# Performance work log

Hardware: AMD Instinct MI355X
Metric: run time of the kernel (lower is better)

Reference implementation:

```python
import jax, jax.numpy as jnp
import numpy as np

B, S, D, H = 64, 512, 1024, 1024


def setup_inputs() -> dict:
    key = jax.random.key(0)
    ks = jax.random.split(key, 7)
    stdv = 1.0 / np.sqrt(H)
    u = lambda k, shape: jax.random.uniform(k, shape, jnp.float32, -stdv, stdv)
    return {
        "inputs": jax.random.normal(ks[0], (B, S, D), jnp.float32),
        "h0": jax.random.normal(ks[1], (1, B, H), jnp.float32),
        "c0": jax.random.normal(ks[2], (1, B, H), jnp.float32),
        "weight_ih": u(ks[3], (4 * H, D)),
        "weight_hh": u(ks[4], (4 * H, H)),
        "bias_ih": u(ks[5], (4 * H,)),
        "bias_hh": u(ks[6], (4 * H,)),
    }


def reference(inputs, h0, c0, weight_ih, weight_hh, bias_ih, bias_hh):
    # Precompute input projection for all timesteps: [B, S, 4H]
    x_proj = jnp.einsum("bsd,gd->bsg", inputs, weight_ih) + bias_ih

    def step(carry, xp):
        h, c = carry  # [B, H]
        gates = xp + h @ weight_hh.T + bias_hh  # [B, 4H]
        i, f, g, o = jnp.split(gates, 4, axis=-1)  # torch gate order: i, f, g(c), o
        i = jax.nn.sigmoid(i)
        f = jax.nn.sigmoid(f)
        g = jnp.tanh(g)
        o = jax.nn.sigmoid(o)
        c = f * c + i * g
        h = o * jnp.tanh(c)
        return (h, c), h

    (hn, cn), outs = jax.lax.scan(step, (h0[0], c0[0]), jnp.swapaxes(x_proj, 0, 1))
    outputs = jnp.swapaxes(outs, 0, 1)  # [B, S, H]
    return outputs, hn[None], cn[None]
```

## Files before the change

### kernel.cpp

```cpp
#include <hip/hip_runtime.h>

typedef __bf16 bf16x8 __attribute__((ext_vector_type(8)));
typedef float f32x4 __attribute__((ext_vector_type(4)));

#define T_STEPS 512

__device__ __forceinline__ float fsig(float v) { return 1.0f / (1.0f + __expf(-v)); }
__device__ __forceinline__ float ftanhf(float v) {
    float a = fminf(fmaxf(v, -15.0f), 15.0f);
    float e = __expf(2.0f * a);
    return (e - 1.0f) / (e + 1.0f);
}
__device__ __forceinline__ unsigned short f2bfu(float f) {
    unsigned u = __float_as_uint(f);
    u += 0x7fffu + ((u >> 16) & 1u);
    return (unsigned short)(u >> 16);
}
__device__ __forceinline__ bf16x8 cvt8(float4 a, float4 b) {
    bf16x8 f;
    f[0] = (__bf16)a.x; f[1] = (__bf16)a.y; f[2] = (__bf16)a.z; f[3] = (__bf16)a.w;
    f[4] = (__bf16)b.x; f[5] = (__bf16)b.y; f[6] = (__bf16)b.z; f[7] = (__bf16)b.w;
    return f;
}

__device__ __forceinline__ void load_hb8(const unsigned short* p, uint4* f) {
    asm volatile(
        "global_load_dwordx4 %0, %8, off sc0 sc1\n\t"
        "global_load_dwordx4 %1, %8, off offset:64 sc0 sc1\n\t"
        "global_load_dwordx4 %2, %8, off offset:128 sc0 sc1\n\t"
        "global_load_dwordx4 %3, %8, off offset:192 sc0 sc1\n\t"
        "global_load_dwordx4 %4, %8, off offset:256 sc0 sc1\n\t"
        "global_load_dwordx4 %5, %8, off offset:320 sc0 sc1\n\t"
        "global_load_dwordx4 %6, %8, off offset:384 sc0 sc1\n\t"
        "global_load_dwordx4 %7, %8, off offset:448 sc0 sc1\n\t"
        "s_waitcnt vmcnt(0)"
        : "=&v"(f[0]), "=&v"(f[1]), "=&v"(f[2]), "=&v"(f[3]),
          "=&v"(f[4]), "=&v"(f[5]), "=&v"(f[6]), "=&v"(f[7])
        : "v"(p)
        : "memory");
}
__device__ __forceinline__ void store_hb(unsigned short* p, unsigned short v) {
    unsigned int vv = v;
    asm volatile("global_store_short %0, %1, off sc0 sc1"
                 :: "v"(p), "v"(vv) : "memory");
}
__device__ __forceinline__ void vm_drain() {
    asm volatile("s_waitcnt vmcnt(0)" ::: "memory");
}

__global__ __launch_bounds__(512, 2) void lstm_persist(
    const float* __restrict__ x, const float* __restrict__ h0,
    const float* __restrict__ c0, const float* __restrict__ w_ih,
    const float* __restrict__ w_hh, const float* __restrict__ b_ih,
    const float* __restrict__ b_hh, float* __restrict__ out,
    unsigned short* __restrict__ hb, int* __restrict__ arrive)
{
    const int tid  = threadIdx.x;
    const int wave = tid >> 6;
    const int lane = tid & 63;
    const int bid  = blockIdx.x;
    const int bg   = bid >> 6;
    const int cg   = bid & 63;
    const int colbase = cg << 4;
    const int batbase = bg << 4;

    __shared__ float xred[2][4][4][4][64];
    __shared__ float hred[4][4][4][64];

    const int quad = lane >> 4;
    const int l15  = lane & 15;

    bf16x8 bw[8][4];
    {
        const float* wsrc = (wave < 4) ? w_ih : w_hh;
        const int koff = (wave & 3) * 256 + quad * 8;
        #pragma unroll
        for (int n = 0; n < 4; ++n) {
            const float* prow = wsrc + (size_t)((n << 10) + colbase + l15) * 1024 + koff;
            #pragma unroll
            for (int kk = 0; kk < 8; ++kk) {
                float4 a = *(const float4*)(prow + kk * 32);
                float4 b = *(const float4*)(prow + kk * 32 + 4);
                bw[kk][n] = cvt8(a, b);
            }
        }
    }

    float creg = 0.0f, bias0 = 0.f, bias1 = 0.f, bias2 = 0.f, bias3 = 0.f;
    int cellcolg = 0, cellb = 0;
    if (tid < 256) {
        const int cl = tid & 63;
        const int cv = tid >> 6;
        const int cellrow = ((cl >> 4) << 2) + cv;
        cellcolg = colbase + (cl & 15);
        cellb    = batbase + cellrow;
        creg  = c0[cellb * 1024 + cellcolg];
        bias0 = b_ih[cellcolg]        + b_hh[cellcolg];
        bias1 = b_ih[1024 + cellcolg] + b_hh[1024 + cellcolg];
        bias2 = b_ih[2048 + cellcolg] + b_hh[2048 + cellcolg];
        bias3 = b_ih[3072 + cellcolg] + b_hh[3072 + cellcolg];
    }

    float* outp = out;
    float* hnp  = out + (size_t)64 * 512 * 1024;
    float* cnp  = hnp + 64 * 1024;

    const int abatch = batbase + l15;

    float4 pa[8], pb[8];

    if (wave < 4) {
        const float* px = x + ((size_t)abatch * 512 + 0) * 1024 + wave * 256 + quad * 8;
        f32x4 xacc[4];
        #pragma unroll
        for (int n = 0; n < 4; ++n) xacc[n] = (f32x4){0.f, 0.f, 0.f, 0.f};
        #pragma unroll
        for (int kk = 0; kk < 8; ++kk) {
            float4 a = *(const float4*)(px + kk * 32);
            float4 b = *(const float4*)(px + kk * 32 + 4);
            bf16x8 af = cvt8(a, b);
            xacc[0] = __builtin_amdgcn_mfma_f32_16x16x32_bf16(af, bw[kk][0], xacc[0], 0, 0, 0);
            xacc[1] = __builtin_amdgcn_mfma_f32_16x16x32_bf16(af, bw[kk][1], xacc[1], 0, 0, 0);
            xacc[2] = __builtin_amdgcn_mfma_f32_16x16x32_bf16(af, bw[kk][2], xacc[2], 0, 0, 0);
            xacc[3] = __builtin_amdgcn_mfma_f32_16x16x32_bf16(af, bw[kk][3], xacc[3], 0, 0, 0);
        }
        #pragma unroll
        for (int n = 0; n < 4; ++n)
            #pragma unroll
            for (int v = 0; v < 4; ++v)
                xred[0][wave][n][v][lane] = xacc[n][v];
        const float* pn = x + ((size_t)abatch * 512 + 1) * 1024 + wave * 256 + quad * 8;
        #pragma unroll
        for (int kk = 0; kk < 8; ++kk) {
            pa[kk] = *(const float4*)(pn + kk * 32);
            pb[kk] = *(const float4*)(pn + kk * 32 + 4);
        }
    }

    for (int t = 0; t < T_STEPS; ++t) {
        if (wave >= 4) {
            f32x4 acc[4];
            #pragma unroll
            for (int n = 0; n < 4; ++n) acc[n] = (f32x4){0.f, 0.f, 0.f, 0.f};

            if (t == 0) {
                const float* ph = h0 + abatch * 1024 + (wave & 3) * 256 + quad * 8;
                #pragma unroll
                for (int kk = 0; kk < 8; ++kk) {
                    float4 a = *(const float4*)(ph + kk * 32);
                    float4 b = *(const float4*)(ph + kk * 32 + 4);
                    bf16x8 af = cvt8(a, b);
                    acc[0] = __builtin_amdgcn_mfma_f32_16x16x32_bf16(af, bw[kk][0], acc[0], 0, 0, 0);
                    acc[1] = __builtin_amdgcn_mfma_f32_16x16x32_bf16(af, bw[kk][1], acc[1], 0, 0, 0);
                    acc[2] = __builtin_amdgcn_mfma_f32_16x16x32_bf16(af, bw[kk][2], acc[2], 0, 0, 0);
                    acc[3] = __builtin_amdgcn_mfma_f32_16x16x32_bf16(af, bw[kk][3], acc[3], 0, 0, 0);
                }
            } else {
                const int* slot = &arrive[(bg << 6) + lane];
                while (__hip_atomic_load(slot, __ATOMIC_RELAXED,
                                         __HIP_MEMORY_SCOPE_AGENT) < t) {
                    __builtin_amdgcn_s_sleep(1);
                }
                const unsigned short* ph = hb + ((t - 1) & 1) * 65536
                                             + abatch * 1024 + (wave & 3) * 256 + quad * 8;
                uint4 fr[8];
                load_hb8(ph, fr);
                #pragma unroll
                for (int kk = 0; kk < 8; ++kk) {
                    union { uint4 u; bf16x8 v; } cc;
                    cc.u = fr[kk];
                    acc[0] = __builtin_amdgcn_mfma_f32_16x16x32_bf16(cc.v, bw[kk][0], acc[0], 0, 0, 0);
                    acc[1] = __builtin_amdgcn_mfma_f32_16x16x32_bf16(cc.v, bw[kk][1], acc[1], 0, 0, 0);
                    acc[2] = __builtin_amdgcn_mfma_f32_16x16x32_bf16(cc.v, bw[kk][2], acc[2], 0, 0, 0);
                    acc[3] = __builtin_amdgcn_mfma_f32_16x16x32_bf16(cc.v, bw[kk][3], acc[3], 0, 0, 0);
                }
            }
            #pragma unroll
            for (int n = 0; n < 4; ++n)
                #pragma unroll
                for (int v = 0; v < 4; ++v)
                    hred[wave - 4][n][v][lane] = acc[n][v];
        }

        __syncthreads();

        float hval = 0.f;
        if (tid < 256) {
            const int cl = tid & 63;
            const int cv = tid >> 6;
            float g0 = bias0, g1 = bias1, g2 = bias2, g3 = bias3;
            #pragma unroll
            for (int w = 0; w < 4; ++w) {
                g0 += xred[t & 1][w][0][cv][cl] + hred[w][0][cv][cl];
                g1 += xred[t & 1][w][1][cv][cl] + hred[w][1][cv][cl];
                g2 += xred[t & 1][w][2][cv][cl] + hred[w][2][cv][cl];
                g3 += xred[t & 1][w][3][cv][cl] + hred[w][3][cv][cl];
            }
            float ig = fsig(g0), fg = fsig(g1), gg = ftanhf(g2), og = fsig(g3);
            creg = fg * creg + ig * gg;
            hval = og * ftanhf(creg);
            store_hb(hb + (t & 1) * 65536 + cellb * 1024 + cellcolg, f2bfu(hval));
            vm_drain();
        }

        __syncthreads();

        if (tid == 0 && t < T_STEPS - 1)
            __hip_atomic_store(&arrive[bid], t + 1, __ATOMIC_RELAXED,
                               __HIP_MEMORY_SCOPE_AGENT);

        if (wave < 4) {
            outp[((size_t)cellb * 512 + t) * 1024 + cellcolg] = hval;
            if (t == T_STEPS - 1) {
                hnp[cellb * 1024 + cellcolg] = hval;
                cnp[cellb * 1024 + cellcolg] = creg;
            }
            if (t < T_STEPS - 1) {
                f32x4 xacc[4];
                #pragma unroll
                for (int n = 0; n < 4; ++n) xacc[n] = (f32x4){0.f, 0.f, 0.f, 0.f};
                #pragma unroll
                for (int kk = 0; kk < 8; ++kk) {
                    bf16x8 af = cvt8(pa[kk], pb[kk]);
                    xacc[0] = __builtin_amdgcn_mfma_f32_16x16x32_bf16(af, bw[kk][0], xacc[0], 0, 0, 0);
                    xacc[1] = __builtin_amdgcn_mfma_f32_16x16x32_bf16(af, bw[kk][1], xacc[1], 0, 0, 0);
                    xacc[2] = __builtin_amdgcn_mfma_f32_16x16x32_bf16(af, bw[kk][2], xacc[2], 0, 0, 0);
                    xacc[3] = __builtin_amdgcn_mfma_f32_16x16x32_bf16(af, bw[kk][3], xacc[3], 0, 0, 0);
                }
                #pragma unroll
                for (int n = 0; n < 4; ++n)
                    #pragma unroll
                    for (int v = 0; v < 4; ++v)
                        xred[(t + 1) & 1][wave][n][v][lane] = xacc[n][v];
                if (t + 2 < T_STEPS) {
                    const float* pn = x + ((size_t)abatch * 512 + (t + 2)) * 1024
                                        + wave * 256 + quad * 8;
                    #pragma unroll
                    for (int kk = 0; kk < 8; ++kk) {
                        pa[kk] = *(const float4*)(pn + kk * 32);
                        pb[kk] = *(const float4*)(pn + kk * 32 + 4);
                    }
                }
            }
        }
    }
}

extern "C" void kernel_launch(void* const* d_in, const int* in_sizes, int n_in,
                              void* d_out, int out_size, void* d_ws, size_t ws_size,
                              hipStream_t stream) {
    const float* x   = (const float*)d_in[0];
    const float* h0  = (const float*)d_in[1];
    const float* c0  = (const float*)d_in[2];
    const float* wih = (const float*)d_in[3];
    const float* whh = (const float*)d_in[4];
    const float* bih = (const float*)d_in[5];
    const float* bhh = (const float*)d_in[6];
    float* out = (float*)d_out;
    unsigned short* hb = (unsigned short*)d_ws;
    int* arrive = (int*)((char*)d_ws + 2 * 65536 * sizeof(unsigned short));
    hipLaunchKernelGGL(lstm_persist, dim3(256), dim3(512), 0, stream,
                       x, h0, c0, wih, whh, bih, bhh, out, hb, arrive);
}
```

Measured before the change: 4.146 ms.

## Replace per-block arrival flags with per-batch-group atomic counter and LDS go flag

Cross-block synchronisation moves from 64 per-block arrival slots, polled by every lane of four waves, to one atomic counter per batch group. Each cell wave increments it after publishing h, and a single wave polls it, then releases the other waves through an LDS flag. The cell update moves to the h-waves so the second __syncthreads before signaling is removed, and the x-waves read h back from LDS to write the outputs. This cuts global polling traffic and shortens the critical path between steps, but adds atomics contention and relies on a memset of the counter before launch.

```diff
diff --git a/kernel.cpp b/kernel.cpp
--- a/kernel.cpp
+++ b/kernel.cpp
@@ -53,7 +53,7 @@
     const float* __restrict__ c0, const float* __restrict__ w_ih,
     const float* __restrict__ w_hh, const float* __restrict__ b_ih,
     const float* __restrict__ b_hh, float* __restrict__ out,
-    unsigned short* __restrict__ hb, int* __restrict__ arrive)
+    unsigned short* __restrict__ hb, int* __restrict__ cnt_base)
 {
     const int tid  = threadIdx.x;
     const int wave = tid >> 6;
@@ -65,10 +65,14 @@
     const int batbase = bg << 4;
 
     __shared__ float xred[2][4][4][4][64];
-    __shared__ float hred[4][4][4][64];
+    __shared__ float hredLDS[4][4][4][64];
+    __shared__ float hout[256];
+    __shared__ int go;
 
     const int quad = lane >> 4;
     const int l15  = lane & 15;
+
+    int* cnt = cnt_base + (bg << 5);
 
     bf16x8 bw[8][4];
     {
@@ -86,20 +90,21 @@
         }
     }
 
+    const int cv = (tid >> 6) & 3;
+    const int cellrow  = ((lane >> 4) << 2) + cv;
+    const int cellcolg = colbase + l15;
+    const int cellb    = batbase + cellrow;
+
     float creg = 0.0f, bias0 = 0.f, bias1 = 0.f, bias2 = 0.f, bias3 = 0.f;
-    int cellcolg = 0, cellb = 0;
-    if (tid < 256) {
-        const int cl = tid & 63;
-        const int cv = tid >> 6;
-        const int cellrow = ((cl >> 4) << 2) + cv;
-        cellcolg = colbase + (cl & 15);
-        cellb    = batbase + cellrow;
+    if (wave >= 4) {
         creg  = c0[cellb * 1024 + cellcolg];
         bias0 = b_ih[cellcolg]        + b_hh[cellcolg];
         bias1 = b_ih[1024 + cellcolg] + b_hh[1024 + cellcolg];
         bias2 = b_ih[2048 + cellcolg] + b_hh[2048 + cellcolg];
         bias3 = b_ih[3072 + cellcolg] + b_hh[3072 + cellcolg];
     }
+    if (tid == 256) __hip_atomic_store(&go, 0, __ATOMIC_RELAXED,
+                                       __HIP_MEMORY_SCOPE_WORKGROUP);
 
     float* outp = out;
     float* hnp  = out + (size_t)64 * 512 * 1024;
@@ -156,10 +161,25 @@
                     acc[3] = __builtin_amdgcn_mfma_f32_16x16x32_bf16(af, bw[kk][3], acc[3], 0, 0, 0);
                 }
             } else {
-                const int* slot = &arrive[(bg << 6) + lane];
-                while (__hip_atomic_load(slot, __ATOMIC_RELAXED,
-                                         __HIP_MEMORY_SCOPE_AGENT) < t) {
-                    __builtin_amdgcn_s_sleep(1);
+                const int target = t << 8;
+                if (wave == 4) {
+                    for (;;) {
+                        int p = 0;
+                        if (lane == 0)
+                            p = __hip_atomic_load(cnt, __ATOMIC_RELAXED,
+                                                  __HIP_MEMORY_SCOPE_AGENT);
+                        p = __builtin_amdgcn_readfirstlane(p);
+                        if (p >= target) break;
+                        __builtin_amdgcn_s_sleep(1);
+                    }
+                    if (lane == 0)
+                        __hip_atomic_store(&go, t, __ATOMIC_RELAXED,
+                                           __HIP_MEMORY_SCOPE_WORKGROUP);
+                } else {
+                    while (__hip_atomic_load(&go, __ATOMIC_RELAXED,
+                                             __HIP_MEMORY_SCOPE_WORKGROUP) < t) {
+                        __builtin_amdgcn_s_sleep(1);
+                    }
                 }
                 const unsigned short* ph = hb + ((t - 1) & 1) * 65536
                                              + abatch * 1024 + (wave & 3) * 256 + quad * 8;
@@ -179,42 +199,43 @@
             for (int n = 0; n < 4; ++n)
                 #pragma unroll
                 for (int v = 0; v < 4; ++v)
-                    hred[wave - 4][n][v][lane] = acc[n][v];
+                    hredLDS[wave - 4][n][v][lane] = acc[n][v];
         }
 
         __syncthreads();
 
-        float hval = 0.f;
-        if (tid < 256) {
-            const int cl = tid & 63;
-            const int cv = tid >> 6;
+        if (wave >= 4) {
+            const int v = wave - 4;
             float g0 = bias0, g1 = bias1, g2 = bias2, g3 = bias3;
+            const int buf = t & 1;
             #pragma unroll
             for (int w = 0; w < 4; ++w) {
-                g0 += xred[t & 1][w][0][cv][cl] + hred[w][0][cv][cl];
-                g1 += xred[t & 1][w][1][cv][cl] + hred[w][1][cv][cl];
-                g2 += xred[t & 1][w][2][cv][cl] + hred[w][2][cv][cl];
-                g3 += xred[t & 1][w][3][cv][cl] + hred[w][3][cv][cl];
+                g0 += xred[buf][w][0][v][lane] + hredLDS[w][0][v][lane];
+                g1 += xred[buf][w][1][v][lane] + hredLDS[w][1][v][lane];
+                g2 += xred[buf][w][2][v][lane] + hredLDS[w][2][v][lane];
+                g3 += xred[buf][w][3][v][lane] + hredLDS[w][3][v][lane];
             }
             float ig = fsig(g0), fg = fsig(g1), gg = ftanhf(g2), og = fsig(g3);
             creg = fg * creg + ig * gg;
-            hval = og * ftanhf(creg);
+            float hval = og * ftanhf(creg);
+            hout[(v << 6) + lane] = hval;
             store_hb(hb + (t & 1) * 65536 + cellb * 1024 + cellcolg, f2bfu(hval));
-            vm_drain();
-        }
-
-        __syncthreads();
-
-        if (tid == 0 && t < T_STEPS - 1)
-            __hip_atomic_store(&arrive[bid], t + 1, __ATOMIC_RELAXED,
-                               __HIP_MEMORY_SCOPE_AGENT);
-
-        if (wave < 4) {
-            outp[((size_t)cellb * 512 + t) * 1024 + cellcolg] = hval;
             if (t == T_STEPS - 1) {
                 hnp[cellb * 1024 + cellcolg] = hval;
                 cnp[cellb * 1024 + cellcolg] = creg;
-            }
+            } else {
+                vm_drain();
+                if (lane == 0)
+                    __hip_atomic_fetch_add(cnt, 1, __ATOMIC_RELAXED,
+                                           __HIP_MEMORY_SCOPE_AGENT);
+            }
+        }
+
+        __syncthreads();
+
+        if (wave < 4) {
+            float hval = hout[tid];
+            outp[((size_t)cellb * 512 + t) * 1024 + cellcolg] = hval;
             if (t < T_STEPS - 1) {
                 f32x4 xacc[4];
                 #pragma unroll
@@ -258,7 +279,8 @@
     const float* bhh = (const float*)d_in[6];
     float* out = (float*)d_out;
     unsigned short* hb = (unsigned short*)d_ws;
-    int* arrive = (int*)((char*)d_ws + 2 * 65536 * sizeof(unsigned short));
+    int* cnt = (int*)((char*)d_ws + 2 * 65536 * sizeof(unsigned short));
+    hipMemsetAsync(cnt, 0, 4 * 128, stream);
     hipLaunchKernelGGL(lstm_persist, dim3(256), dim3(512), 0, stream,
-                       x, h0, c0, wih, whh, bih, bhh, out, hb, arrive);
-}
+                       x, h0, c0, wih, whh, bih, bhh, out, hb, cnt);
+}
```

After: 5.378 ms. +29.7%, slower.
